# Kernel optimization log

Measured on AMD Instinct MI355X. Metric: run time of the kernel, lower is better.

Reference implementation:

```python
import jax, jax.numpy as jnp
import numpy as np

H = W = 32
V = 1.5  # gaussian sigma used by the original _gussin(1.5)

def _gaussian_table():
    # gus[p, x, y] with p = i*32 + k, matching the original nested loops.
    r = np.arange(H, dtype=np.float64)
    d = (r[:, None, None, None] - r[None, None, :, None]) ** 2 \
        + (r[None, :, None, None] - r[None, None, None, :]) ** 2  # [i,k,x,y]
    g = np.exp(-d / (2.0 * V * V)) / (2.0 * np.pi * V * V)
    g = g.reshape(H * W, H, W)
    g = g / g.sum(axis=(1, 2), keepdims=True)  # per-position boundary normalization
    return jnp.asarray(g, dtype=jnp.float32)

_GUS = _gaussian_table()  # [1024, 32, 32]

def setup_inputs() -> dict:
    key = jax.random.key(0)
    ks = jax.random.split(key, 5)
    c, r = 1024, 16
    return {
        "x": jax.random.normal(ks[0], (1, c, H, W), jnp.float32),
        "se_w1": jax.random.normal(ks[1], (c // r, c), jnp.float32) * 0.03,
        "se_b1": jnp.zeros((c // r,), jnp.float32),
        "se_w2": jax.random.normal(ks[2], (c, c // r), jnp.float32) * 0.1,
        "se_b2": jnp.zeros((c,), jnp.float32),
        "conv_w": jax.random.normal(ks[3], (c, 2 * c), jnp.float32) * 0.02,
        "bn_gamma": jnp.ones((c,), jnp.float32),
        "bn_beta": jnp.zeros((c,), jnp.float32),
        "bn_mean": jnp.zeros((c,), jnp.float32),
        "bn_var": jnp.ones((c,), jnp.float32),
    }

def reference(x, se_w1, se_b1, se_w2, se_b2, conv_w, bn_gamma, bn_beta, bn_mean, bn_var):
    b, c, h, w = x.shape  # b == 1, h == w == 32 (hardcoded by the gaussian table)
    # ---- SE block ----
    y = x.mean(axis=(2, 3))                              # [b, c]
    y = jax.nn.relu(y @ se_w1.T + se_b1)                 # [b, c//r]
    y = jax.nn.sigmoid(y @ se_w2.T + se_b2)              # [b, c]
    x = x * y[:, :, None, None]
    # ---- gaussian spatial pooling (algebraic form of the O(H^2 W^2 C) expand) ----
    # x_spatial[c, p] = sum_{h,w} x[c,h,w] * gus[p,h,w]
    x_spatial = jnp.einsum('chw,phw->cp', x[0], _GUS).reshape(c, h, w)
    # ---- 3x3 local softmax attention on sigmoid features ----
    xr = jax.nn.sigmoid(x)                               # [1, c, h, w]
    xp = jnp.pad(xr, ((0, 0), (0, 0), (1, 1), (1, 1)))
    # torch F.unfold ordering: feature index = c_idx*9 + kh*3 + kw
    patches = jnp.stack([xp[:, :, i:i + h, j:j + w]
                         for i in range(3) for j in range(3)], axis=2)  # [1, c, 9, h, w]
    u = patches.reshape(c * 9, h * w).T                  # [hw, c*9]
    # faithful to the original reshape(hw, 3, 3, c) (reinterprets the c*9 layout)
    x3 = u.reshape(h * w, 3, 3, c)
    x1 = xr[0].transpose(1, 2, 0).reshape(h * w, 1, 1, c)
    logits = (x1 * x3).sum(-1).reshape(h * w, 9)         # [hw, 9]
    attn = jax.nn.softmax(logits, axis=1).reshape(h * w, 3, 3)
    x_range = jnp.einsum('pij,pijc->cp', attn, x3).reshape(c, h, w)
    # ---- fuse: 1x1 conv (no bias) + eval-mode BatchNorm + ReLU ----
    cat = jnp.concatenate([x_range, x_spatial], axis=0).reshape(b, 2 * c, h, w)
    out = jnp.einsum('oc,bchw->bohw', conv_w, cat)
    inv = jax.lax.rsqrt(bn_var + 1e-5)
    out = (out - bn_mean[None, :, None, None]) * (inv * bn_gamma)[None, :, None, None] \
          + bn_beta[None, :, None, None]
    return jax.nn.relu(out)
```

## Files before the change

kernel.cpp:

```cpp
#include <hip/hip_runtime.h>
#include <hip/hip_bf16.h>


typedef __attribute__((ext_vector_type(8))) short v8s;
typedef __attribute__((ext_vector_type(4))) float v4f;

__device__ __forceinline__ float sigmoidf_(float v) {
    return 1.f / (1.f + __expf(-v));
}
__device__ __forceinline__ unsigned short f2bf(float f) {
    unsigned u = __float_as_uint(f);
    u += 0x7fffu + ((u >> 16) & 1u);
    return (unsigned short)(u >> 16);
}
__device__ __forceinline__ float bf2f(unsigned short s) {
    return __uint_as_float(((unsigned)s) << 16);
}

__global__ __launch_bounds__(256) void k_A(const float* __restrict__ x,
                                           const float* __restrict__ w1,
                                           const float* __restrict__ gamma,
                                           const float* __restrict__ beta,
                                           const float* __restrict__ mu,
                                           const float* __restrict__ var,
                                           unsigned short* __restrict__ U,
                                           float* __restrict__ zpart,
                                           float* __restrict__ bnsc,
                                           float* __restrict__ bnsh) {
    __shared__ unsigned short Gb[32 * 48];
    __shared__ unsigned short Xs[4][32 * 48];
    __shared__ unsigned short Ts[4][32 * 48];
    __shared__ float ms4[4];
    int tid = threadIdx.x, bx = blockIdx.x;
    int wv = tid >> 6, lane = tid & 63;
    {
        int row = tid >> 3, col0 = (tid & 7) << 2;
        float e[4], s = 0.f;
        #pragma unroll
        for (int j = 0; j < 4; ++j) {
            float d = (float)(row - (col0 + j));
            e[j] = __expf(-d * d / 4.5f);
            s += e[j];
        }
        s += __shfl_xor(s, 4, 8);
        s += __shfl_xor(s, 2, 8);
        s += __shfl_xor(s, 1, 8);
        float is = 1.f / s;
        uint2 pk;
        pk.x = (unsigned)f2bf(e[0] * is) | ((unsigned)f2bf(e[1] * is) << 16);
        pk.y = (unsigned)f2bf(e[2] * is) | ((unsigned)f2bf(e[3] * is) << 16);
        *(uint2*)&Gb[row * 48 + col0] = pk;
    }
    int c = (bx << 2) + wv;
    if (lane == 0) {
        float iv = rsqrtf(var[c] + 1e-5f);
        float sc = iv * gamma[c];
        bnsc[c] = sc;
        bnsh[c] = beta[c] - mu[c] * sc;
    }
    const float* xp = x + (size_t)c * 1024;
    float4 vj[4];
    float s = 0.f;
    #pragma unroll
    for (int j = 0; j < 4; ++j) {
        vj[j] = *(const float4*)(xp + (j << 8) + (lane << 2));
        s += vj[j].x + vj[j].y + vj[j].z + vj[j].w;
    }
    #pragma unroll
    for (int o = 32; o; o >>= 1) s += __shfl_down(s, o);
    if (lane == 0) ms4[wv] = s * (1.f / 1024.f);
    #pragma unroll
    for (int j = 0; j < 4; ++j) {
        int h = (j << 3) + (lane >> 3);
        int w0 = (lane & 7) << 2;
        uint2 pk;
        pk.x = (unsigned)f2bf(vj[j].x) | ((unsigned)f2bf(vj[j].y) << 16);
        pk.y = (unsigned)f2bf(vj[j].z) | ((unsigned)f2bf(vj[j].w) << 16);
        *(uint2*)&Xs[wv][h * 48 + w0] = pk;
    }
    __syncthreads();
    int colf = lane & 15, quad = lane >> 4;
    v8s ga[2], xbv[2];
    #pragma unroll
    for (int mi = 0; mi < 2; ++mi)
        ga[mi] = *(const v8s*)&Gb[(mi * 16 + colf) * 48 + quad * 8];
    #pragma unroll
    for (int ni = 0; ni < 2; ++ni)
        xbv[ni] = *(const v8s*)&Xs[wv][(ni * 16 + colf) * 48 + quad * 8];
    v4f c1[2][2];
    #pragma unroll
    for (int mi = 0; mi < 2; ++mi)
        #pragma unroll
        for (int ni = 0; ni < 2; ++ni) {
            c1[mi][ni] = (v4f){0.f, 0.f, 0.f, 0.f};
            c1[mi][ni] = __builtin_amdgcn_mfma_f32_16x16x32_bf16(ga[mi], xbv[ni], c1[mi][ni], 0, 0, 0);
        }
    #pragma unroll
    for (int mi = 0; mi < 2; ++mi)
        #pragma unroll
        for (int ni = 0; ni < 2; ++ni)
            #pragma unroll
            for (int r = 0; r < 4; ++r)
                Ts[wv][(mi * 16 + quad * 4 + r) * 48 + ni * 16 + colf] = f2bf(c1[mi][ni][r]);
    __syncthreads();
    v8s tb[2];
    #pragma unroll
    for (int ni = 0; ni < 2; ++ni)
        tb[ni] = *(const v8s*)&Ts[wv][(ni * 16 + colf) * 48 + quad * 8];
    v4f c2[2][2];
    #pragma unroll
    for (int mi = 0; mi < 2; ++mi)
        #pragma unroll
        for (int ni = 0; ni < 2; ++ni) {
            c2[mi][ni] = (v4f){0.f, 0.f, 0.f, 0.f};
            c2[mi][ni] = __builtin_amdgcn_mfma_f32_16x16x32_bf16(ga[mi], tb[ni], c2[mi][ni], 0, 0, 0);
        }
    #pragma unroll
    for (int mi = 0; mi < 2; ++mi)
        #pragma unroll
        for (int ni = 0; ni < 2; ++ni)
            #pragma unroll
            for (int r = 0; r < 4; ++r)
                U[(size_t)c * 1024 + (mi * 16 + quad * 4 + r) * 32 + ni * 16 + colf] =
                    f2bf(c2[mi][ni][r]);
    if (wv == 0) {
        float4 wr = *(const float4*)(w1 + (size_t)lane * 1024 + (bx << 2));
        zpart[lane * 256 + bx] = wr.x * ms4[0] + wr.y * ms4[1]
                               + wr.z * ms4[2] + wr.w * ms4[3];
    }
}

__global__ __launch_bounds__(256) void k_prep(const float* __restrict__ x,
                                              const float* __restrict__ zpart,
                                              const float* __restrict__ b1,
                                              const float* __restrict__ w2,
                                              const float* __restrict__ b2,
                                              const unsigned short* __restrict__ U,
                                              unsigned short* __restrict__ xrb,
                                              unsigned short* __restrict__ Bt) {
    __shared__ float y1s[64];
    __shared__ float y2s[64];
    __shared__ float T1[64][65];
    __shared__ float T2[64][65];
    int tid = threadIdx.x;
    int p0 = blockIdx.x << 6, c0 = blockIdx.y << 6;
    {
        int j = tid >> 2, q = tid & 3;
        const float4* zp = (const float4*)(zpart + j * 256 + q * 64);
        float s = 0.f;
        #pragma unroll
        for (int i = 0; i < 16; ++i) {
            float4 v = zp[i];
            s += v.x + v.y + v.z + v.w;
        }
        s += __shfl_down(s, 2, 4);
        s += __shfl_down(s, 1, 4);
        if (q == 0) y1s[j] = fmaxf(s + b1[j], 0.f);
    }
    __syncthreads();
    {
        int ci = tid >> 2, sub = tid & 3;
        float s = 0.f;
        const float* w2r = w2 + (size_t)(c0 + ci) * 64 + sub * 16;
        #pragma unroll
        for (int i = 0; i < 4; ++i) {
            float4 wv4 = *(const float4*)(w2r + (i << 2));
            float4 yv4 = *(const float4*)&y1s[sub * 16 + (i << 2)];
            s += wv4.x * yv4.x + wv4.y * yv4.y + wv4.z * yv4.z + wv4.w * yv4.w;
        }
        s += __shfl_down(s, 2, 4);
        s += __shfl_down(s, 1, 4);
        if (sub == 0) y2s[ci] = sigmoidf_(s + b2[c0 + ci]);
    }
    __syncthreads();
    #pragma unroll
    for (int i = 0; i < 4; ++i) {
        int idx = tid + (i << 8);
        int row = idx >> 4;
        int col = (idx & 15) << 2;
        float sc = y2s[row];
        float4 v = *(const float4*)(x + (size_t)(c0 + row) * 1024 + p0 + col);
        uint2 pu = *(const uint2*)(U + (size_t)(c0 + row) * 1024 + p0 + col);
        T1[col + 0][row] = sigmoidf_(v.x * sc);
        T1[col + 1][row] = sigmoidf_(v.y * sc);
        T1[col + 2][row] = sigmoidf_(v.z * sc);
        T1[col + 3][row] = sigmoidf_(v.w * sc);
        T2[col + 0][row] = bf2f((unsigned short)(pu.x & 0xffffu)) * sc;
        T2[col + 1][row] = bf2f((unsigned short)(pu.x >> 16)) * sc;
        T2[col + 2][row] = bf2f((unsigned short)(pu.y & 0xffffu)) * sc;
        T2[col + 3][row] = bf2f((unsigned short)(pu.y >> 16)) * sc;
    }
    __syncthreads();
    #pragma unroll
    for (int i = 0; i < 4; ++i) {
        int idx = tid + (i << 8);
        int prow = idx >> 4;
        int cc = (idx & 15) << 2;
        uint2 pk1, pk2;
        pk1.x = (unsigned)f2bf(T1[prow][cc + 0]) | ((unsigned)f2bf(T1[prow][cc + 1]) << 16);
        pk1.y = (unsigned)f2bf(T1[prow][cc + 2]) | ((unsigned)f2bf(T1[prow][cc + 3]) << 16);
        pk2.x = (unsigned)f2bf(T2[prow][cc + 0]) | ((unsigned)f2bf(T2[prow][cc + 1]) << 16);
        pk2.y = (unsigned)f2bf(T2[prow][cc + 2]) | ((unsigned)f2bf(T2[prow][cc + 3]) << 16);
        *(uint2*)(xrb + (size_t)(p0 + prow) * 1024 + c0 + cc) = pk1;
        *(uint2*)(Bt + (size_t)(p0 + prow) * 2048 + 1024 + c0 + cc) = pk2;
    }
}

__global__ __launch_bounds__(256) void k_attn(const unsigned short* __restrict__ xrb,
                                              const float* __restrict__ W,
                                              unsigned short* __restrict__ Wb,
                                              unsigned short* __restrict__ Bt) {
    __shared__ struct { unsigned short val[9216]; float part[9][4]; } sm;
    int tid = threadIdx.x;
    int p = blockIdx.x;
    int wv = tid >> 6, lane = tid & 63;
    int h = p >> 5, w = p & 31;
    {
        int e0 = (p << 11) + (tid << 2);
        float4 v0 = *(const float4*)(W + e0);
        float4 v1 = *(const float4*)(W + e0 + 1024);
        uint2 pk0, pk1;
        pk0.x = (unsigned)f2bf(v0.x) | ((unsigned)f2bf(v0.y) << 16);
        pk0.y = (unsigned)f2bf(v0.z) | ((unsigned)f2bf(v0.w) << 16);
        pk1.x = (unsigned)f2bf(v1.x) | ((unsigned)f2bf(v1.y) << 16);
        pk1.y = (unsigned)f2bf(v1.z) | ((unsigned)f2bf(v1.w) << 16);
        *(uint2*)(Wb + e0) = pk0;
        *(uint2*)(Wb + e0 + 1024) = pk1;
    }
    float ctr[4];
    #pragma unroll
    for (int rem = 0; rem < 9; ++rem) {
        int dh = rem / 3 - 1, dw = rem % 3 - 1;
        bool ok = ((unsigned)(h + dh) < 32u) && ((unsigned)(w + dw) < 32u);
        uint2 v = make_uint2(0u, 0u);
        if (ok)
            v = *(const uint2*)(xrb + (size_t)((h + dh) * 32 + (w + dw)) * 1024 + 4 * tid);
        unsigned short e0 = (unsigned short)(v.x & 0xffffu);
        unsigned short e1 = (unsigned short)(v.x >> 16);
        unsigned short e2 = (unsigned short)(v.y & 0xffffu);
        unsigned short e3 = (unsigned short)(v.y >> 16);
        sm.val[(4 * tid + 0) * 9 + rem] = e0;
        sm.val[(4 * tid + 1) * 9 + rem] = e1;
        sm.val[(4 * tid + 2) * 9 + rem] = e2;
        sm.val[(4 * tid + 3) * 9 + rem] = e3;
        if (rem == 4) {
            ctr[0] = bf2f(e0); ctr[1] = bf2f(e1); ctr[2] = bf2f(e2); ctr[3] = bf2f(e3);
        }
    }
    __syncthreads();
    float vvq[9][4], lg[9];
    #pragma unroll
    for (int q = 0; q < 9; ++q) {
        uint2 pk = *(const uint2*)&sm.val[(q << 10) + 4 * tid];
        vvq[q][0] = bf2f((unsigned short)(pk.x & 0xffffu));
        vvq[q][1] = bf2f((unsigned short)(pk.x >> 16));
        vvq[q][2] = bf2f((unsigned short)(pk.y & 0xffffu));
        vvq[q][3] = bf2f((unsigned short)(pk.y >> 16));
        lg[q] = ctr[0] * vvq[q][0] + ctr[1] * vvq[q][1]
              + ctr[2] * vvq[q][2] + ctr[3] * vvq[q][3];
    }
    #pragma unroll
    for (int q = 0; q < 9; ++q) {
        float s = lg[q];
        #pragma unroll
        for (int o = 32; o; o >>= 1) s += __shfl_down(s, o);
        if (lane == 0) sm.part[q][wv] = s;
    }
    __syncthreads();
    float a9[9], mx = -3.4e38f;
    #pragma unroll
    for (int q = 0; q < 9; ++q) {
        a9[q] = sm.part[q][0] + sm.part[q][1] + sm.part[q][2] + sm.part[q][3];
        mx = fmaxf(mx, a9[q]);
    }
    float se = 0.f;
    #pragma unroll
    for (int q = 0; q < 9; ++q) { a9[q] = __expf(a9[q] - mx); se += a9[q]; }
    float inv = 1.f / se;
    float o4[4] = {0.f, 0.f, 0.f, 0.f};
    #pragma unroll
    for (int q = 0; q < 9; ++q) {
        float a = a9[q] * inv;
        #pragma unroll
        for (int j = 0; j < 4; ++j) o4[j] += a * vvq[q][j];
    }
    uint2 pk;
    pk.x = (unsigned)f2bf(o4[0]) | ((unsigned)f2bf(o4[1]) << 16);
    pk.y = (unsigned)f2bf(o4[2]) | ((unsigned)f2bf(o4[3]) << 16);
    *(uint2*)(Bt + (size_t)p * 2048 + 4 * tid) = pk;
}

__global__ __launch_bounds__(512) void k_main(
    const unsigned short* __restrict__ A, const unsigned short* __restrict__ B,
    float* __restrict__ outF,
    const float* __restrict__ bnsc, const float* __restrict__ bnsh) {
    __shared__ unsigned short As[2][64 * 136];
    __shared__ unsigned short Bs[2][64 * 136];
    const int K = 2048;
    int tid = threadIdx.x;
    int bid = blockIdx.x;
    int xcd = bid & 7, idx = bid >> 3;
    int by = ((xcd >> 1) << 2) + (idx >> 3);
    int bxn = ((xcd & 1) << 3) + (idx & 7);
    int m0 = by << 6, n0 = bxn << 6;
    int wv = tid >> 6, lane = tid & 63;
    int wm = wv & 3, wn = wv >> 2;
    int col = lane & 15, quad = lane >> 4;
    int srow = tid >> 3;
    int schunk = tid & 7;
    v4f acc[2];
    acc[0] = (v4f){0.f, 0.f, 0.f, 0.f};
    acc[1] = (v4f){0.f, 0.f, 0.f, 0.f};

    const float4* pa = (const float4*)(A + (size_t)(m0 + srow) * K + schunk * 8);
    const float4* pb = (const float4*)(B + (size_t)(n0 + srow) * K + schunk * 8);
    float4 ra0 = pa[0], ra1 = pa[8], rb0 = pb[0], rb1 = pb[8];
    *(float4*)&As[0][srow * 136 + schunk * 8] = ra0;
    *(float4*)&As[0][srow * 136 + schunk * 8 + 64] = ra1;
    *(float4*)&Bs[0][srow * 136 + schunk * 8] = rb0;
    *(float4*)&Bs[0][srow * 136 + schunk * 8 + 64] = rb1;
    for (int it = 0; it < 16; ++it) {
        __syncthreads();
        int cur = it & 1;
        if (it + 1 < 16) {
            int k0 = (it + 1) << 7;
            pa = (const float4*)(A + (size_t)(m0 + srow) * K + k0 + schunk * 8);
            pb = (const float4*)(B + (size_t)(n0 + srow) * K + k0 + schunk * 8);
            ra0 = pa[0]; ra1 = pa[8];
            rb0 = pb[0]; rb1 = pb[8];
        }
        #pragma unroll
        for (int ks = 0; ks < 4; ++ks) {
            int kg = ks * 4 + quad;
            int rA = wm * 16 + col;
            int rB = wn * 32 + col;
            v8s a  = *(const v8s*)&As[cur][rA * 136 + kg * 8];
            v8s b0 = *(const v8s*)&Bs[cur][rB * 136 + kg * 8];
            v8s b1 = *(const v8s*)&Bs[cur][(rB + 16) * 136 + kg * 8];
            acc[0] = __builtin_amdgcn_mfma_f32_16x16x32_bf16(a, b0, acc[0], 0, 0, 0);
            acc[1] = __builtin_amdgcn_mfma_f32_16x16x32_bf16(a, b1, acc[1], 0, 0, 0);
        }
        if (it + 1 < 16) {
            int nxt = cur ^ 1;
            *(float4*)&As[nxt][srow * 136 + schunk * 8] = ra0;
            *(float4*)&As[nxt][srow * 136 + schunk * 8 + 64] = ra1;
            *(float4*)&Bs[nxt][srow * 136 + schunk * 8] = rb0;
            *(float4*)&Bs[nxt][srow * 136 + schunk * 8 + 64] = rb1;
        }
    }
    #pragma unroll
    for (int ni = 0; ni < 2; ++ni) {
        int mb = m0 + wm * 16 + quad * 4;
        int nn = n0 + wn * 32 + ni * 16 + col;
        #pragma unroll
        for (int r = 0; r < 4; ++r) {
            int mm = mb + r;
            float sc = bnsc[mm];
            float sh = bnsh[mm];
            outF[((size_t)mm << 10) + nn] = fmaxf(fmaf(acc[ni][r], sc, sh), 0.f);
        }
    }
}

extern "C" void kernel_launch(void* const* d_in, const int* in_sizes, int n_in,
                              void* d_out, int out_size, void* d_ws, size_t ws_size,
                              hipStream_t stream) {
    const float* x     = (const float*)d_in[0];
    const float* w1    = (const float*)d_in[1];
    const float* b1    = (const float*)d_in[2];
    const float* w2    = (const float*)d_in[3];
    const float* b2    = (const float*)d_in[4];
    const float* cw    = (const float*)d_in[5];
    const float* gamma = (const float*)d_in[6];
    const float* beta  = (const float*)d_in[7];
    const float* mu    = (const float*)d_in[8];
    const float* var   = (const float*)d_in[9];
    float* wsf = (float*)d_ws;
    unsigned short* Wb  = (unsigned short*)wsf;
    unsigned short* Bt  = (unsigned short*)(wsf + (1 << 20));
    unsigned short* xrb = (unsigned short*)(wsf + (2 << 20));
    unsigned short* U   = (unsigned short*)(wsf + (2 << 20) + (1 << 19));
    float* zpart = wsf + (3 << 20);
    float* bnsc  = zpart + 16384;
    float* bnsh  = bnsc + 1024;
    float* out  = (float*)d_out;

    k_A    <<<256, 256, 0, stream>>>(x, w1, gamma, beta, mu, var, U, zpart, bnsc, bnsh);
    k_prep <<<dim3(16, 16), 256, 0, stream>>>(x, zpart, b1, w2, b2, U, xrb, Bt);
    k_attn <<<1024, 256, 0, stream>>>(xrb, cw, Wb, Bt);
    k_main <<<256, 512, 0, stream>>>(Wb, Bt, out, bnsc, bnsh);
}
```

Baseline: 113.2 us.

## Merge prep and attention kernels with flag-based inter-block synchronization

Fuses k_prep and k_attn into a single 768-block launch. The first 256 blocks do the SE/transpose prep and publish a per-block completion flag, while the remaining blocks convert the conv weights to bf16 and spin-wait on all 256 flags before running the local attention for two positions each. The intent is to remove one kernel launch and boundary, and to overlap the weight conversion with the prep work. The cost is spin-wait synchronization, which assumes the prep blocks get scheduled before or alongside the waiting blocks; otherwise it could deadlock.

```diff
diff --git a/kernel.cpp b/kernel.cpp
--- a/kernel.cpp
+++ b/kernel.cpp
@@ -4,6 +4,8 @@
 
 typedef __attribute__((ext_vector_type(8))) short v8s;
 typedef __attribute__((ext_vector_type(4))) float v4f;
+
+#define DONE_MAGIC 0x17C0DE5Au
 
 __device__ __forceinline__ float sigmoidf_(float v) {
     return 1.f / (1.f + __expf(-v));
@@ -26,13 +28,16 @@
                                            unsigned short* __restrict__ U,
                                            float* __restrict__ zpart,
                                            float* __restrict__ bnsc,
-                                           float* __restrict__ bnsh) {
+                                           float* __restrict__ bnsh,
+                                           unsigned int* __restrict__ flags) {
     __shared__ unsigned short Gb[32 * 48];
     __shared__ unsigned short Xs[4][32 * 48];
     __shared__ unsigned short Ts[4][32 * 48];
     __shared__ float ms4[4];
     int tid = threadIdx.x, bx = blockIdx.x;
     int wv = tid >> 6, lane = tid & 63;
+    if (tid == 0)
+        __hip_atomic_store(&flags[bx], 0u, __ATOMIC_RELAXED, __HIP_MEMORY_SCOPE_AGENT);
     {
         int row = tid >> 3, col0 = (tid & 7) << 2;
         float e[4], s = 0.f;
@@ -130,164 +135,193 @@
     }
 }
 
-__global__ __launch_bounds__(256) void k_prep(const float* __restrict__ x,
-                                              const float* __restrict__ zpart,
-                                              const float* __restrict__ b1,
-                                              const float* __restrict__ w2,
-                                              const float* __restrict__ b2,
-                                              const unsigned short* __restrict__ U,
-                                              unsigned short* __restrict__ xrb,
-                                              unsigned short* __restrict__ Bt) {
-    __shared__ float y1s[64];
-    __shared__ float y2s[64];
-    __shared__ float T1[64][65];
-    __shared__ float T2[64][65];
+struct PrepS {
+    float y1s[64];
+    float y2s[64];
+    float T1[64][65];
+    float T2[64][65];
+};
+struct AttnS {
+    unsigned short val[9216];
+    float part[9][4];
+};
+union __align__(16) SMemPA {
+    PrepS p;
+    AttnS a;
+};
+
+__global__ __launch_bounds__(256, 4) void k_pa(const float* __restrict__ x,
+                                               const float* __restrict__ zpart,
+                                               const float* __restrict__ b1,
+                                               const float* __restrict__ w2,
+                                               const float* __restrict__ b2,
+                                               const unsigned short* __restrict__ U,
+                                               const float* __restrict__ W,
+                                               unsigned short* __restrict__ Wb,
+                                               unsigned short* __restrict__ xrb,
+                                               unsigned short* __restrict__ Bt,
+                                               unsigned int* __restrict__ flags) {
+    __shared__ SMemPA sm;
     int tid = threadIdx.x;
-    int p0 = blockIdx.x << 6, c0 = blockIdx.y << 6;
-    {
-        int j = tid >> 2, q = tid & 3;
-        const float4* zp = (const float4*)(zpart + j * 256 + q * 64);
-        float s = 0.f;
-        #pragma unroll
-        for (int i = 0; i < 16; ++i) {
-            float4 v = zp[i];
-            s += v.x + v.y + v.z + v.w;
-        }
-        s += __shfl_down(s, 2, 4);
-        s += __shfl_down(s, 1, 4);
-        if (q == 0) y1s[j] = fmaxf(s + b1[j], 0.f);
-    }
-    __syncthreads();
-    {
-        int ci = tid >> 2, sub = tid & 3;
-        float s = 0.f;
-        const float* w2r = w2 + (size_t)(c0 + ci) * 64 + sub * 16;
+    int bid = blockIdx.x;
+    int wv = tid >> 6, lane = tid & 63;
+    if (bid < 256) {
+        int p0 = (bid & 15) << 6, c0 = (bid >> 4) << 6;
+        {
+            int j = tid >> 2, q = tid & 3;
+            const float4* zp = (const float4*)(zpart + j * 256 + q * 64);
+            float s = 0.f;
+            #pragma unroll
+            for (int i = 0; i < 16; ++i) {
+                float4 v = zp[i];
+                s += v.x + v.y + v.z + v.w;
+            }
+            s += __shfl_down(s, 2, 4);
+            s += __shfl_down(s, 1, 4);
+            if (q == 0) sm.p.y1s[j] = fmaxf(s + b1[j], 0.f);
+        }
+        __syncthreads();
+        {
+            int ci = tid >> 2, sub = tid & 3;
+            float s = 0.f;
+            const float* w2r = w2 + (size_t)(c0 + ci) * 64 + sub * 16;
+            #pragma unroll
+            for (int i = 0; i < 4; ++i) {
+                float4 wv4 = *(const float4*)(w2r + (i << 2));
+                float4 yv4 = *(const float4*)&sm.p.y1s[sub * 16 + (i << 2)];
+                s += wv4.x * yv4.x + wv4.y * yv4.y + wv4.z * yv4.z + wv4.w * yv4.w;
+            }
+            s += __shfl_down(s, 2, 4);
+            s += __shfl_down(s, 1, 4);
+            if (sub == 0) sm.p.y2s[ci] = sigmoidf_(s + b2[c0 + ci]);
+        }
+        __syncthreads();
         #pragma unroll
         for (int i = 0; i < 4; ++i) {
-            float4 wv4 = *(const float4*)(w2r + (i << 2));
-            float4 yv4 = *(const float4*)&y1s[sub * 16 + (i << 2)];
-            s += wv4.x * yv4.x + wv4.y * yv4.y + wv4.z * yv4.z + wv4.w * yv4.w;
-        }
-        s += __shfl_down(s, 2, 4);
-        s += __shfl_down(s, 1, 4);
-        if (sub == 0) y2s[ci] = sigmoidf_(s + b2[c0 + ci]);
-    }
-    __syncthreads();
-    #pragma unroll
-    for (int i = 0; i < 4; ++i) {
-        int idx = tid + (i << 8);
-        int row = idx >> 4;
-        int col = (idx & 15) << 2;
-        float sc = y2s[row];
-        float4 v = *(const float4*)(x + (size_t)(c0 + row) * 1024 + p0 + col);
-        uint2 pu = *(const uint2*)(U + (size_t)(c0 + row) * 1024 + p0 + col);
-        T1[col + 0][row] = sigmoidf_(v.x * sc);
-        T1[col + 1][row] = sigmoidf_(v.y * sc);
-        T1[col + 2][row] = sigmoidf_(v.z * sc);
-        T1[col + 3][row] = sigmoidf_(v.w * sc);
-        T2[col + 0][row] = bf2f((unsigned short)(pu.x & 0xffffu)) * sc;
-        T2[col + 1][row] = bf2f((unsigned short)(pu.x >> 16)) * sc;
-        T2[col + 2][row] = bf2f((unsigned short)(pu.y & 0xffffu)) * sc;
-        T2[col + 3][row] = bf2f((unsigned short)(pu.y >> 16)) * sc;
-    }
-    __syncthreads();
-    #pragma unroll
-    for (int i = 0; i < 4; ++i) {
-        int idx = tid + (i << 8);
-        int prow = idx >> 4;
-        int cc = (idx & 15) << 2;
-        uint2 pk1, pk2;
-        pk1.x = (unsigned)f2bf(T1[prow][cc + 0]) | ((unsigned)f2bf(T1[prow][cc + 1]) << 16);
-        pk1.y = (unsigned)f2bf(T1[prow][cc + 2]) | ((unsigned)f2bf(T1[prow][cc + 3]) << 16);
-        pk2.x = (unsigned)f2bf(T2[prow][cc + 0]) | ((unsigned)f2bf(T2[prow][cc + 1]) << 16);
-        pk2.y = (unsigned)f2bf(T2[prow][cc + 2]) | ((unsigned)f2bf(T2[prow][cc + 3]) << 16);
-        *(uint2*)(xrb + (size_t)(p0 + prow) * 1024 + c0 + cc) = pk1;
-        *(uint2*)(Bt + (size_t)(p0 + prow) * 2048 + 1024 + c0 + cc) = pk2;
-    }
-}
-
-__global__ __launch_bounds__(256) void k_attn(const unsigned short* __restrict__ xrb,
-                                              const float* __restrict__ W,
-                                              unsigned short* __restrict__ Wb,
-                                              unsigned short* __restrict__ Bt) {
-    __shared__ struct { unsigned short val[9216]; float part[9][4]; } sm;
-    int tid = threadIdx.x;
-    int p = blockIdx.x;
-    int wv = tid >> 6, lane = tid & 63;
-    int h = p >> 5, w = p & 31;
-    {
-        int e0 = (p << 11) + (tid << 2);
-        float4 v0 = *(const float4*)(W + e0);
-        float4 v1 = *(const float4*)(W + e0 + 1024);
-        uint2 pk0, pk1;
-        pk0.x = (unsigned)f2bf(v0.x) | ((unsigned)f2bf(v0.y) << 16);
-        pk0.y = (unsigned)f2bf(v0.z) | ((unsigned)f2bf(v0.w) << 16);
-        pk1.x = (unsigned)f2bf(v1.x) | ((unsigned)f2bf(v1.y) << 16);
-        pk1.y = (unsigned)f2bf(v1.z) | ((unsigned)f2bf(v1.w) << 16);
-        *(uint2*)(Wb + e0) = pk0;
-        *(uint2*)(Wb + e0 + 1024) = pk1;
-    }
-    float ctr[4];
-    #pragma unroll
-    for (int rem = 0; rem < 9; ++rem) {
-        int dh = rem / 3 - 1, dw = rem % 3 - 1;
-        bool ok = ((unsigned)(h + dh) < 32u) && ((unsigned)(w + dw) < 32u);
-        uint2 v = make_uint2(0u, 0u);
-        if (ok)
-            v = *(const uint2*)(xrb + (size_t)((h + dh) * 32 + (w + dw)) * 1024 + 4 * tid);
-        unsigned short e0 = (unsigned short)(v.x & 0xffffu);
-        unsigned short e1 = (unsigned short)(v.x >> 16);
-        unsigned short e2 = (unsigned short)(v.y & 0xffffu);
-        unsigned short e3 = (unsigned short)(v.y >> 16);
-        sm.val[(4 * tid + 0) * 9 + rem] = e0;
-        sm.val[(4 * tid + 1) * 9 + rem] = e1;
-        sm.val[(4 * tid + 2) * 9 + rem] = e2;
-        sm.val[(4 * tid + 3) * 9 + rem] = e3;
-        if (rem == 4) {
-            ctr[0] = bf2f(e0); ctr[1] = bf2f(e1); ctr[2] = bf2f(e2); ctr[3] = bf2f(e3);
-        }
-    }
-    __syncthreads();
-    float vvq[9][4], lg[9];
-    #pragma unroll
-    for (int q = 0; q < 9; ++q) {
-        uint2 pk = *(const uint2*)&sm.val[(q << 10) + 4 * tid];
-        vvq[q][0] = bf2f((unsigned short)(pk.x & 0xffffu));
-        vvq[q][1] = bf2f((unsigned short)(pk.x >> 16));
-        vvq[q][2] = bf2f((unsigned short)(pk.y & 0xffffu));
-        vvq[q][3] = bf2f((unsigned short)(pk.y >> 16));
-        lg[q] = ctr[0] * vvq[q][0] + ctr[1] * vvq[q][1]
-              + ctr[2] * vvq[q][2] + ctr[3] * vvq[q][3];
-    }
-    #pragma unroll
-    for (int q = 0; q < 9; ++q) {
-        float s = lg[q];
-        #pragma unroll
-        for (int o = 32; o; o >>= 1) s += __shfl_down(s, o);
-        if (lane == 0) sm.part[q][wv] = s;
-    }
-    __syncthreads();
-    float a9[9], mx = -3.4e38f;
-    #pragma unroll
-    for (int q = 0; q < 9; ++q) {
-        a9[q] = sm.part[q][0] + sm.part[q][1] + sm.part[q][2] + sm.part[q][3];
-        mx = fmaxf(mx, a9[q]);
-    }
-    float se = 0.f;
-    #pragma unroll
-    for (int q = 0; q < 9; ++q) { a9[q] = __expf(a9[q] - mx); se += a9[q]; }
-    float inv = 1.f / se;
-    float o4[4] = {0.f, 0.f, 0.f, 0.f};
-    #pragma unroll
-    for (int q = 0; q < 9; ++q) {
-        float a = a9[q] * inv;
-        #pragma unroll
-        for (int j = 0; j < 4; ++j) o4[j] += a * vvq[q][j];
-    }
-    uint2 pk;
-    pk.x = (unsigned)f2bf(o4[0]) | ((unsigned)f2bf(o4[1]) << 16);
-    pk.y = (unsigned)f2bf(o4[2]) | ((unsigned)f2bf(o4[3]) << 16);
-    *(uint2*)(Bt + (size_t)p * 2048 + 4 * tid) = pk;
+            int idx = tid + (i << 8);
+            int row = idx >> 4;
+            int col = (idx & 15) << 2;
+            float sc = sm.p.y2s[row];
+            float4 v = *(const float4*)(x + (size_t)(c0 + row) * 1024 + p0 + col);
+            uint2 pu = *(const uint2*)(U + (size_t)(c0 + row) * 1024 + p0 + col);
+            sm.p.T1[col + 0][row] = sigmoidf_(v.x * sc);
+            sm.p.T1[col + 1][row] = sigmoidf_(v.y * sc);
+            sm.p.T1[col + 2][row] = sigmoidf_(v.z * sc);
+            sm.p.T1[col + 3][row] = sigmoidf_(v.w * sc);
+            sm.p.T2[col + 0][row] = bf2f((unsigned short)(pu.x & 0xffffu)) * sc;
+            sm.p.T2[col + 1][row] = bf2f((unsigned short)(pu.x >> 16)) * sc;
+            sm.p.T2[col + 2][row] = bf2f((unsigned short)(pu.y & 0xffffu)) * sc;
+            sm.p.T2[col + 3][row] = bf2f((unsigned short)(pu.y >> 16)) * sc;
+        }
+        __syncthreads();
+        #pragma unroll
+        for (int i = 0; i < 4; ++i) {
+            int idx = tid + (i << 8);
+            int prow = idx >> 4;
+            int cc = (idx & 15) << 2;
+            uint2 pk1, pk2;
+            pk1.x = (unsigned)f2bf(sm.p.T1[prow][cc + 0]) | ((unsigned)f2bf(sm.p.T1[prow][cc + 1]) << 16);
+            pk1.y = (unsigned)f2bf(sm.p.T1[prow][cc + 2]) | ((unsigned)f2bf(sm.p.T1[prow][cc + 3]) << 16);
+            pk2.x = (unsigned)f2bf(sm.p.T2[prow][cc + 0]) | ((unsigned)f2bf(sm.p.T2[prow][cc + 1]) << 16);
+            pk2.y = (unsigned)f2bf(sm.p.T2[prow][cc + 2]) | ((unsigned)f2bf(sm.p.T2[prow][cc + 3]) << 16);
+            *(uint2*)(xrb + (size_t)(p0 + prow) * 1024 + c0 + cc) = pk1;
+            *(uint2*)(Bt + (size_t)(p0 + prow) * 2048 + 1024 + c0 + cc) = pk2;
+        }
+        __syncthreads();
+        if (tid == 0) {
+            __threadfence();
+            __hip_atomic_store(&flags[bid], DONE_MAGIC, __ATOMIC_RELAXED,
+                               __HIP_MEMORY_SCOPE_AGENT);
+        }
+    } else {
+        int ab = bid - 256;
+        {
+            int e0 = (ab << 12) + (tid << 2);
+            #pragma unroll
+            for (int k = 0; k < 4; ++k) {
+                float4 v = *(const float4*)(W + e0 + (k << 10));
+                uint2 pk;
+                pk.x = (unsigned)f2bf(v.x) | ((unsigned)f2bf(v.y) << 16);
+                pk.y = (unsigned)f2bf(v.z) | ((unsigned)f2bf(v.w) << 16);
+                *(uint2*)(Wb + e0 + (k << 10)) = pk;
+            }
+        }
+        while (__hip_atomic_load(&flags[tid], __ATOMIC_RELAXED,
+                                 __HIP_MEMORY_SCOPE_AGENT) != DONE_MAGIC)
+            __builtin_amdgcn_s_sleep(32);
+        __syncthreads();
+        if (tid == 0) __threadfence();
+        __syncthreads();
+        #pragma unroll 1
+        for (int ip = 0; ip < 2; ++ip) {
+            int p = (ab << 1) + ip;
+            int h = p >> 5, w = p & 31;
+            float ctr[4];
+            #pragma unroll
+            for (int rem = 0; rem < 9; ++rem) {
+                int dh = rem / 3 - 1, dw = rem % 3 - 1;
+                bool ok = ((unsigned)(h + dh) < 32u) && ((unsigned)(w + dw) < 32u);
+                uint2 v = make_uint2(0u, 0u);
+                if (ok)
+                    v = *(const uint2*)(xrb + (size_t)((h + dh) * 32 + (w + dw)) * 1024 + 4 * tid);
+                unsigned short e0 = (unsigned short)(v.x & 0xffffu);
+                unsigned short e1 = (unsigned short)(v.x >> 16);
+                unsigned short e2 = (unsigned short)(v.y & 0xffffu);
+                unsigned short e3 = (unsigned short)(v.y >> 16);
+                sm.a.val[(4 * tid + 0) * 9 + rem] = e0;
+                sm.a.val[(4 * tid + 1) * 9 + rem] = e1;
+                sm.a.val[(4 * tid + 2) * 9 + rem] = e2;
+                sm.a.val[(4 * tid + 3) * 9 + rem] = e3;
+                if (rem == 4) {
+                    ctr[0] = bf2f(e0); ctr[1] = bf2f(e1);
+                    ctr[2] = bf2f(e2); ctr[3] = bf2f(e3);
+                }
+            }
+            __syncthreads();
+            float vvq[9][4], lg[9];
+            #pragma unroll
+            for (int q = 0; q < 9; ++q) {
+                uint2 pk = *(const uint2*)&sm.a.val[(q << 10) + 4 * tid];
+                vvq[q][0] = bf2f((unsigned short)(pk.x & 0xffffu));
+                vvq[q][1] = bf2f((unsigned short)(pk.x >> 16));
+                vvq[q][2] = bf2f((unsigned short)(pk.y & 0xffffu));
+                vvq[q][3] = bf2f((unsigned short)(pk.y >> 16));
+                lg[q] = ctr[0] * vvq[q][0] + ctr[1] * vvq[q][1]
+                      + ctr[2] * vvq[q][2] + ctr[3] * vvq[q][3];
+            }
+            #pragma unroll
+            for (int q = 0; q < 9; ++q) {
+                float s = lg[q];
+                #pragma unroll
+                for (int o = 32; o; o >>= 1) s += __shfl_down(s, o);
+                if (lane == 0) sm.a.part[q][wv] = s;
+            }
+            __syncthreads();
+            float a9[9], mx = -3.4e38f;
+            #pragma unroll
+            for (int q = 0; q < 9; ++q) {
+                a9[q] = sm.a.part[q][0] + sm.a.part[q][1]
+                      + sm.a.part[q][2] + sm.a.part[q][3];
+                mx = fmaxf(mx, a9[q]);
+            }
+            float se = 0.f;
+            #pragma unroll
+            for (int q = 0; q < 9; ++q) { a9[q] = __expf(a9[q] - mx); se += a9[q]; }
+            float inv = 1.f / se;
+            float o4[4] = {0.f, 0.f, 0.f, 0.f};
+            #pragma unroll
+            for (int q = 0; q < 9; ++q) {
+                float a = a9[q] * inv;
+                #pragma unroll
+                for (int j = 0; j < 4; ++j) o4[j] += a * vvq[q][j];
+            }
+            uint2 pk;
+            pk.x = (unsigned)f2bf(o4[0]) | ((unsigned)f2bf(o4[1]) << 16);
+            pk.y = (unsigned)f2bf(o4[2]) | ((unsigned)f2bf(o4[3]) << 16);
+            *(uint2*)(Bt + (size_t)p * 2048 + 4 * tid) = pk;
+            __syncthreads();
+        }
+    }
 }
 
 __global__ __launch_bounds__(512) void k_main(
@@ -383,10 +417,10 @@
     float* zpart = wsf + (3 << 20);
     float* bnsc  = zpart + 16384;
     float* bnsh  = bnsc + 1024;
+    unsigned int* flags = (unsigned int*)(bnsh + 1024);
     float* out  = (float*)d_out;
 
-    k_A    <<<256, 256, 0, stream>>>(x, w1, gamma, beta, mu, var, U, zpart, bnsc, bnsh);
-    k_prep <<<dim3(16, 16), 256, 0, stream>>>(x, zpart, b1, w2, b2, U, xrb, Bt);
-    k_attn <<<1024, 256, 0, stream>>>(xrb, cw, Wb, Bt);
+    k_A    <<<256, 256, 0, stream>>>(x, w1, gamma, beta, mu, var, U, zpart, bnsc, bnsh, flags);
+    k_pa   <<<768, 256, 0, stream>>>(x, zpart, b1, w2, b2, U, cw, Wb, xrb, Bt, flags);
     k_main <<<256, 512, 0, stream>>>(Wb, Bt, out, bnsc, bnsh);
 }
```

New measurement: 134.1 us. 1.18x slower.
